# Optimization experiments

Measured on AMD Instinct MI355X. Metric: run time of the kernel, lower is better.

The kernel has to match this reference:

```python
import jax, jax.numpy as jnp
import numpy as np

IN_FEATURES = 2048
OUT_FEATURES = 4096
NUM_SHIFTS = 10  # perms


def setup_inputs() -> dict:
    key = jax.random.key(0)
    kx, kw = jax.random.split(key)
    x = jax.random.normal(kx, (4, 2048, IN_FEATURES), dtype=jnp.float32)
    # nn.Linear weight: (out_features, in_features), Kaiming-uniform-ish init
    bound = 1.0 / np.sqrt(IN_FEATURES)
    W = jax.random.uniform(kw, (OUT_FEATURES, IN_FEATURES), dtype=jnp.float32,
                           minval=-bound, maxval=bound)
    return {"x": x, "W": W}


def _combined_weight(W):
    # Wt: (in, out). Sum of all weight variants; sum_i(x @ W_i) == x @ sum_i(W_i).
    Wt = W.T
    Weff = Wt + jnp.flip(Wt, axis=0) + jnp.flip(Wt, axis=1)
    for i in range(NUM_SHIFTS // 2):
        Weff = Weff + jnp.roll(Wt, shift=i + 1, axis=1)
        Weff = Weff + jnp.roll(Wt, shift=i + 1, axis=0)
    return Weff  # (in, out)


def reference(x, W):
    # reg_out (x @ W.T) + flipped + rolled variants, collapsed into one GEMM
    Weff = _combined_weight(W)
    return jnp.einsum('bsi,io->bso', x, Weff)
```

## Files before the change

kernel.cpp:

```cpp
#include <hip/hip_runtime.h>
#include <hip/hip_bf16.h>
#include <stdint.h>

#define M_DIM 8192
#define K_DIM 2048
#define N_DIM 4096
#define BM 256
#define BN 256
#define BK 64
#define NT (K_DIM / BK)
#define NITER (NT / 2)

typedef __attribute__((ext_vector_type(8))) short bf16x8;
typedef __attribute__((ext_vector_type(4))) float f32x4;

__device__ __forceinline__ unsigned short f2bfu(float f) {
    __hip_bfloat16 h = __float2bfloat16(f);
    return __builtin_bit_cast(unsigned short, h);
}

__global__ __launch_bounds__(256) void prep_fused(const float* __restrict__ x,
                                                  const float* __restrict__ W,
                                                  unsigned short* __restrict__ xb,
                                                  unsigned short* __restrict__ wt) {
    const int bid = blockIdx.x;
    if (bid < N_DIM / 2) {
        __shared__ float row0[K_DIM];
        __shared__ float row1[K_DIM];
        const int o0 = bid * 2;
        const float* w0 = W + (size_t)o0 * K_DIM;
        const float* w1 = W + (size_t)(o0 + 1) * K_DIM;
#pragma unroll
        for (int t = 0; t < 2; ++t) {
            ((float4*)row0)[threadIdx.x + 256 * t] = ((const float4*)w0)[threadIdx.x + 256 * t];
            ((float4*)row1)[threadIdx.x + 256 * t] = ((const float4*)w1)[threadIdx.x + 256 * t];
        }
        __syncthreads();

        const float* rF0 = W + (size_t)(N_DIM - 1 - o0) * K_DIM;
        const float* rF1 = W + (size_t)(N_DIM - 2 - o0) * K_DIM;
        const float* rm1 = W + (size_t)((o0 - 1) & (N_DIM - 1)) * K_DIM;
        const float* rm2 = W + (size_t)((o0 - 2) & (N_DIM - 1)) * K_DIM;
        const float* rm3 = W + (size_t)((o0 - 3) & (N_DIM - 1)) * K_DIM;
        const float* rm4 = W + (size_t)((o0 - 4) & (N_DIM - 1)) * K_DIM;
        const float* rm5 = W + (size_t)((o0 - 5) & (N_DIM - 1)) * K_DIM;
        unsigned short* wo0 = wt + (size_t)o0 * K_DIM;
        unsigned short* wo1 = wo0 + K_DIM;

#pragma unroll
        for (int t = 0; t < 2; ++t) {
            const int i0 = (threadIdx.x + 256 * t) * 4;
            const float4 vF0 = *(const float4*)(rF0 + i0);
            const float4 vF1 = *(const float4*)(rF1 + i0);
            const float4 v1  = *(const float4*)(rm1 + i0);
            const float4 v2  = *(const float4*)(rm2 + i0);
            const float4 v3  = *(const float4*)(rm3 + i0);
            const float4 v4  = *(const float4*)(rm4 + i0);
            const float4 v5  = *(const float4*)(rm5 + i0);
            ushort4 ov0, ov1;
#pragma unroll
            for (int j = 0; j < 4; ++j) {
                const int i = i0 + j;
                float s0 = row0[i] + row0[K_DIM - 1 - i]
                         + row0[(i - 1) & (K_DIM - 1)] + row0[(i - 2) & (K_DIM - 1)]
                         + row0[(i - 3) & (K_DIM - 1)] + row0[(i - 4) & (K_DIM - 1)]
                         + row0[(i - 5) & (K_DIM - 1)];
                s0 += (&vF0.x)[j] + (&v1.x)[j] + (&v2.x)[j]
                    + (&v3.x)[j] + (&v4.x)[j] + (&v5.x)[j];
                (&ov0.x)[j] = f2bfu(s0);

                float s1 = row1[i] + row1[K_DIM - 1 - i]
                         + row1[(i - 1) & (K_DIM - 1)] + row1[(i - 2) & (K_DIM - 1)]
                         + row1[(i - 3) & (K_DIM - 1)] + row1[(i - 4) & (K_DIM - 1)]
                         + row1[(i - 5) & (K_DIM - 1)];
                s1 += (&vF1.x)[j] + row0[i] + (&v1.x)[j] + (&v2.x)[j]
                    + (&v3.x)[j] + (&v4.x)[j];
                (&ov1.x)[j] = f2bfu(s1);
            }
            *(ushort4*)(wo0 + i0) = ov0;
            *(ushort4*)(wo1 + i0) = ov1;
        }
    } else {
        const int idx = (bid - N_DIM / 2) * 256 + threadIdx.x;
        float4 v = ((const float4*)x)[idx];
        ushort4 o;
        o.x = f2bfu(v.x); o.y = f2bfu(v.y); o.z = f2bfu(v.z); o.w = f2bfu(v.w);
        ((ushort4*)xb)[idx] = o;
    }
}

__global__ __launch_bounds__(512, 2) void gemm8p(const unsigned short* __restrict__ Ab,
                                                 const unsigned short* __restrict__ Bt,
                                                 float* __restrict__ C) {
    __shared__ __align__(16) char smem[2 * 65536];

    const int tid  = threadIdx.x;
    const int wave = tid >> 6;
    const int lane = tid & 63;

    const int cpx = 256 >> 3;
    const int wg  = ((int)blockIdx.x & 7) * cpx + ((int)blockIdx.x >> 3);

    const int wr = wave >> 2;
    const int wc = wave & 3;

    const int srow = tid >> 3;
    const int lsw  = (lane & 7) ^ ((lane >> 3) & 7);

    const int r16  = lane & 15;
    const int x7   = lane & 7;
    const int ksl0 = (((lane >> 4)    ) ^ x7) * 16;
    const int ksl1 = (((lane >> 4) | 4) ^ x7) * 16;
    const int aRow = (wr * 128 + r16) * 128;
    const int bRow = (wc * 64  + r16) * 128 + 32768;
    const int crow = (lane >> 4) * 4;
    const int ccol = lane & 15;

    f32x4  acc[8][4];
    bf16x8 b[4][2];
    const unsigned short* gA0;
    const unsigned short* gB0;

#define STAGE_HALF(gbase, opoff, h, t, p) do {                                              \
    char* lds_ = smem + (p) * 65536 + (opoff) + (h) * 16384 + wave * 1024;                  \
    const unsigned short* g_ = (gbase) + (size_t)((h) * 128) * K_DIM + (t) * BK;            \
    __builtin_amdgcn_global_load_lds(                                                        \
        (const __attribute__((address_space(1))) unsigned int*)g_,                           \
        (__attribute__((address_space(3))) unsigned int*)lds_, 16, 0, 0);                    \
    __builtin_amdgcn_global_load_lds(                                                        \
        (const __attribute__((address_space(1))) unsigned int*)(g_ + (size_t)64 * K_DIM),    \
        (__attribute__((address_space(3))) unsigned int*)(lds_ + 8192), 16, 0, 0);           \
} while (0)

#define PHASE(P, Q, STAGE_STMT, VM_STMT) do {                                               \
    const char* base_ = smem + (P) * 65536;                                                 \
    bf16x8 a_[2][2];                                                                        \
    a_[0][0] = *(const bf16x8*)(base_ + aRow + (Q) * 4096 + ksl0);                          \
    a_[0][1] = *(const bf16x8*)(base_ + aRow + (Q) * 4096 + ksl1);                          \
    a_[1][0] = *(const bf16x8*)(base_ + aRow + (Q) * 4096 + 2048 + ksl0);                   \
    a_[1][1] = *(const bf16x8*)(base_ + aRow + (Q) * 4096 + 2048 + ksl1);                   \
    STAGE_STMT;                                                                             \
    __builtin_amdgcn_s_barrier();                                                           \
    asm volatile("s_waitcnt lgkmcnt(0)" ::: "memory");                                      \
    __builtin_amdgcn_sched_barrier(0);                                                      \
    __builtin_amdgcn_s_setprio(1);                                                          \
    _Pragma("unroll")                                                                       \
    for (int fm = 0; fm < 2; ++fm)                                                          \
        _Pragma("unroll")                                                                   \
        for (int fn = 0; fn < 4; ++fn) {                                                    \
            acc[(Q)*2 + fm][fn] = __builtin_amdgcn_mfma_f32_16x16x32_bf16(                  \
                a_[fm][0], b[fn][0], acc[(Q)*2 + fm][fn], 0, 0, 0);                         \
            acc[(Q)*2 + fm][fn] = __builtin_amdgcn_mfma_f32_16x16x32_bf16(                  \
                a_[fm][1], b[fn][1], acc[(Q)*2 + fm][fn], 0, 0, 0);                         \
        }                                                                                   \
    __builtin_amdgcn_s_setprio(0);                                                          \
    VM_STMT;                                                                                \
    __builtin_amdgcn_s_barrier();                                                           \
} while (0)

#define FN_CLUSTER(Q, FN) do {                                                              \
    _Pragma("unroll")                                                                       \
    for (int fm = 0; fm < 2; ++fm) {                                                        \
        acc[(Q)*2 + fm][FN] = __builtin_amdgcn_mfma_f32_16x16x32_bf16(                      \
            a_[fm][0], b[FN][0], acc[(Q)*2 + fm][FN], 0, 0, 0);                             \
        acc[(Q)*2 + fm][FN] = __builtin_amdgcn_mfma_f32_16x16x32_bf16(                      \
            a_[fm][1], b[FN][1], acc[(Q)*2 + fm][FN], 0, 0, 0);                             \
    }                                                                                       \
} while (0)

#define PHASE_B(P, Q, STAGE_STMT, VM_STMT) do {                                             \
    const char* base_ = smem + (P) * 65536;                                                 \
    bf16x8 a_[2][2];                                                                        \
    a_[0][0] = *(const bf16x8*)(base_ + aRow + (Q) * 4096 + ksl0);                          \
    a_[0][1] = *(const bf16x8*)(base_ + aRow + (Q) * 4096 + ksl1);                          \
    a_[1][0] = *(const bf16x8*)(base_ + aRow + (Q) * 4096 + 2048 + ksl0);                   \
    a_[1][1] = *(const bf16x8*)(base_ + aRow + (Q) * 4096 + 2048 + ksl1);                   \
    b[0][0] = *(const bf16x8*)(base_ + bRow + ksl0);                                        \
    b[0][1] = *(const bf16x8*)(base_ + bRow + ksl1);                                        \
    __builtin_amdgcn_sched_barrier(0);                                                      \
    b[1][0] = *(const bf16x8*)(base_ + bRow + 2048 + ksl0);                                 \
    b[1][1] = *(const bf16x8*)(base_ + bRow + 2048 + ksl1);                                 \
    __builtin_amdgcn_sched_barrier(0);                                                      \
    b[2][0] = *(const bf16x8*)(base_ + bRow + 4096 + ksl0);                                 \
    b[2][1] = *(const bf16x8*)(base_ + bRow + 4096 + ksl1);                                 \
    __builtin_amdgcn_sched_barrier(0);                                                      \
    b[3][0] = *(const bf16x8*)(base_ + bRow + 6144 + ksl0);                                 \
    b[3][1] = *(const bf16x8*)(base_ + bRow + 6144 + ksl1);                                 \
    __builtin_amdgcn_sched_barrier(0);                                                      \
    STAGE_STMT;                                                                             \
    __builtin_amdgcn_s_barrier();                                                           \
    asm volatile("s_waitcnt lgkmcnt(6)" ::: "memory");                                      \
    __builtin_amdgcn_sched_barrier(0);                                                      \
    __builtin_amdgcn_s_setprio(1);                                                          \
    FN_CLUSTER(Q, 0);                                                                       \
    __builtin_amdgcn_sched_barrier(0);                                                      \
    asm volatile("s_waitcnt lgkmcnt(4)" ::: "memory");                                      \
    __builtin_amdgcn_sched_barrier(0);                                                      \
    FN_CLUSTER(Q, 1);                                                                       \
    __builtin_amdgcn_sched_barrier(0);                                                      \
    asm volatile("s_waitcnt lgkmcnt(2)" ::: "memory");                                      \
    __builtin_amdgcn_sched_barrier(0);                                                      \
    FN_CLUSTER(Q, 2);                                                                       \
    __builtin_amdgcn_sched_barrier(0);                                                      \
    asm volatile("s_waitcnt lgkmcnt(0)" ::: "memory");                                      \
    __builtin_amdgcn_sched_barrier(0);                                                      \
    FN_CLUSTER(Q, 3);                                                                       \
    __builtin_amdgcn_s_setprio(0);                                                          \
    VM_STMT;                                                                                \
    __builtin_amdgcn_s_barrier();                                                           \
} while (0)

#define PROLOGUE() do {                                                                     \
    STAGE_HALF(gB0, 32768, 0, 0, 0);                                                        \
    STAGE_HALF(gB0, 32768, 1, 0, 0);                                                        \
    STAGE_HALF(gA0, 0,     0, 0, 0);                                                        \
    STAGE_HALF(gA0, 0,     1, 0, 0);                                                        \
    STAGE_HALF(gB0, 32768, 0, 1, 1);                                                        \
    STAGE_HALF(gB0, 32768, 1, 1, 1);                                                        \
    STAGE_HALF(gA0, 0,     0, 1, 1);                                                        \
    asm volatile("s_waitcnt vmcnt(6)" ::: "memory");                                        \
    __builtin_amdgcn_s_barrier();                                                           \
} while (0)

#define KLOOP() do {                                                                        \
    for (int u = 0; u < NITER; ++u) {                                                       \
        const bool last = (u == NITER - 1);                                                 \
        const int  t1 = 2 * u + 1, t2 = 2 * u + 2, t3 = 2 * u + 3;                          \
        PHASE_B(0, 0, { STAGE_HALF(gA0, 0, 1, t1, 1); }, {});                               \
        PHASE(0, 1, { if (!last) STAGE_HALF(gB0, 32768, 0, t2, 0); }, {});                  \
        PHASE(0, 2, { if (!last) STAGE_HALF(gB0, 32768, 1, t2, 0); }, {});                  \
        PHASE(0, 3, { if (!last) STAGE_HALF(gA0, 0, 0, t2, 0); },                           \
              { if (last) asm volatile("s_waitcnt vmcnt(0)" ::: "memory");                  \
                else      asm volatile("s_waitcnt vmcnt(6)" ::: "memory"); });              \
        PHASE_B(1, 0, { if (!last) STAGE_HALF(gA0, 0, 1, t2, 0); }, {});                    \
        PHASE(1, 1, { if (!last) STAGE_HALF(gB0, 32768, 0, t3, 1); }, {});                  \
        PHASE(1, 2, { if (!last) STAGE_HALF(gB0, 32768, 1, t3, 1); }, {});                  \
        PHASE(1, 3, { if (!last) STAGE_HALF(gA0, 0, 0, t3, 1); },                           \
              { if (!last) asm volatile("s_waitcnt vmcnt(6)" ::: "memory"); });             \
    }                                                                                       \
} while (0)

#define CSTORE(Cb) do {                                                                     \
    _Pragma("unroll")                                                                       \
    for (int fm = 0; fm < 8; ++fm)                                                          \
        _Pragma("unroll")                                                                   \
        for (int fn = 0; fn < 4; ++fn)                                                      \
            _Pragma("unroll")                                                               \
            for (int r = 0; r < 4; ++r)                                                     \
                (Cb)[(size_t)(fm * 16 + r) * N_DIM + fn * 16] = acc[fm][fn][r];             \
} while (0)

#define ZERO_ACC() do {                                                                     \
    _Pragma("unroll")                                                                       \
    for (int i_ = 0; i_ < 8; ++i_)                                                          \
        _Pragma("unroll")                                                                   \
        for (int j_ = 0; j_ < 4; ++j_)                                                      \
            acc[i_][j_] = (f32x4){0.f, 0.f, 0.f, 0.f};                                      \
} while (0)

    int bm0 = (wg >> 4) * BM;
    int bn0 = (wg & 15) * BN;
    gA0 = Ab + (size_t)(bm0 + srow) * K_DIM + lsw * 8;
    gB0 = Bt + (size_t)(bn0 + srow) * K_DIM + lsw * 8;
    float* Cb0 = C + (size_t)(bm0 + wr * 128 + crow) * N_DIM + (bn0 + wc * 64 + ccol);

    PROLOGUE();
    ZERO_ACC();
    KLOOP();

    bm0 += 4096;
    gA0 = Ab + (size_t)(bm0 + srow) * K_DIM + lsw * 8;
    float* Cb1 = C + (size_t)(bm0 + wr * 128 + crow) * N_DIM + (bn0 + wc * 64 + ccol);

    PROLOGUE();
    CSTORE(Cb0);
    ZERO_ACC();
    KLOOP();
    CSTORE(Cb1);

#undef CSTORE
#undef ZERO_ACC
#undef KLOOP
#undef PROLOGUE
#undef PHASE_B
#undef FN_CLUSTER
#undef PHASE
#undef STAGE_HALF
}

extern "C" void kernel_launch(void* const* d_in, const int* in_sizes, int n_in,
                              void* d_out, int out_size, void* d_ws, size_t ws_size,
                              hipStream_t stream) {
    const float* x = (const float*)d_in[0];
    const float* W = (const float*)d_in[1];
    float* out = (float*)d_out;

    unsigned short* xb = (unsigned short*)d_ws;
    unsigned short* wt = (unsigned short*)((char*)d_ws + (size_t)M_DIM * K_DIM * 2);

    const int cvt_blocks = (M_DIM * K_DIM) / 4 / 256;
    prep_fused<<<N_DIM / 2 + cvt_blocks, 256, 0, stream>>>(x, W, xb, wt);

    gemm8p<<<256, 512, 0, stream>>>(xb, wt, out);
}
```

Before: 164.0 us.

## Fuse x fp32-to-bf16 conversion into GEMM A-tile loading via registers

Removes the separate pass that converted x to bf16 in a workspace. The GEMM now loads fp32 A tiles into registers, converts them to bf16 and writes them into swizzled LDS, with the load issue and LDS write placed across the pipeline phases. This avoids writing and re-reading a bf16 copy of x. In exchange it doubles A-side global read bytes and adds VGPR pressure and conversion ALU work inside the GEMM loop. It also drops the staggered B-fragment loads of the old PHASE_B variant.

```diff
diff --git a/kernel.cpp b/kernel.cpp
--- a/kernel.cpp
+++ b/kernel.cpp
@@ -19,77 +19,66 @@
     return __builtin_bit_cast(unsigned short, h);
 }
 
-__global__ __launch_bounds__(256) void prep_fused(const float* __restrict__ x,
-                                                  const float* __restrict__ W,
-                                                  unsigned short* __restrict__ xb,
-                                                  unsigned short* __restrict__ wt) {
-    const int bid = blockIdx.x;
-    if (bid < N_DIM / 2) {
-        __shared__ float row0[K_DIM];
-        __shared__ float row1[K_DIM];
-        const int o0 = bid * 2;
-        const float* w0 = W + (size_t)o0 * K_DIM;
-        const float* w1 = W + (size_t)(o0 + 1) * K_DIM;
+__global__ __launch_bounds__(256) void prep_weff(const float* __restrict__ W,
+                                                 unsigned short* __restrict__ wt) {
+    __shared__ float row0[K_DIM];
+    __shared__ float row1[K_DIM];
+    const int o0 = blockIdx.x * 2;
+    const float* w0 = W + (size_t)o0 * K_DIM;
+    const float* w1 = W + (size_t)(o0 + 1) * K_DIM;
 #pragma unroll
-        for (int t = 0; t < 2; ++t) {
-            ((float4*)row0)[threadIdx.x + 256 * t] = ((const float4*)w0)[threadIdx.x + 256 * t];
-            ((float4*)row1)[threadIdx.x + 256 * t] = ((const float4*)w1)[threadIdx.x + 256 * t];
+    for (int t = 0; t < 2; ++t) {
+        ((float4*)row0)[threadIdx.x + 256 * t] = ((const float4*)w0)[threadIdx.x + 256 * t];
+        ((float4*)row1)[threadIdx.x + 256 * t] = ((const float4*)w1)[threadIdx.x + 256 * t];
+    }
+    __syncthreads();
+
+    const float* rF0 = W + (size_t)(N_DIM - 1 - o0) * K_DIM;
+    const float* rF1 = W + (size_t)(N_DIM - 2 - o0) * K_DIM;
+    const float* rm1 = W + (size_t)((o0 - 1) & (N_DIM - 1)) * K_DIM;
+    const float* rm2 = W + (size_t)((o0 - 2) & (N_DIM - 1)) * K_DIM;
+    const float* rm3 = W + (size_t)((o0 - 3) & (N_DIM - 1)) * K_DIM;
+    const float* rm4 = W + (size_t)((o0 - 4) & (N_DIM - 1)) * K_DIM;
+    const float* rm5 = W + (size_t)((o0 - 5) & (N_DIM - 1)) * K_DIM;
+    unsigned short* wo0 = wt + (size_t)o0 * K_DIM;
+    unsigned short* wo1 = wo0 + K_DIM;
+
+#pragma unroll
+    for (int t = 0; t < 2; ++t) {
+        const int i0 = (threadIdx.x + 256 * t) * 4;
+        const float4 vF0 = *(const float4*)(rF0 + i0);
+        const float4 vF1 = *(const float4*)(rF1 + i0);
+        const float4 v1  = *(const float4*)(rm1 + i0);
+        const float4 v2  = *(const float4*)(rm2 + i0);
+        const float4 v3  = *(const float4*)(rm3 + i0);
+        const float4 v4  = *(const float4*)(rm4 + i0);
+        const float4 v5  = *(const float4*)(rm5 + i0);
+        ushort4 ov0, ov1;
+#pragma unroll
+        for (int j = 0; j < 4; ++j) {
+            const int i = i0 + j;
+            float s0 = row0[i] + row0[K_DIM - 1 - i]
+                     + row0[(i - 1) & (K_DIM - 1)] + row0[(i - 2) & (K_DIM - 1)]
+                     + row0[(i - 3) & (K_DIM - 1)] + row0[(i - 4) & (K_DIM - 1)]
+                     + row0[(i - 5) & (K_DIM - 1)];
+            s0 += (&vF0.x)[j] + (&v1.x)[j] + (&v2.x)[j]
+                + (&v3.x)[j] + (&v4.x)[j] + (&v5.x)[j];
+            (&ov0.x)[j] = f2bfu(s0);
+
+            float s1 = row1[i] + row1[K_DIM - 1 - i]
+                     + row1[(i - 1) & (K_DIM - 1)] + row1[(i - 2) & (K_DIM - 1)]
+                     + row1[(i - 3) & (K_DIM - 1)] + row1[(i - 4) & (K_DIM - 1)]
+                     + row1[(i - 5) & (K_DIM - 1)];
+            s1 += (&vF1.x)[j] + row0[i] + (&v1.x)[j] + (&v2.x)[j]
+                + (&v3.x)[j] + (&v4.x)[j];
+            (&ov1.x)[j] = f2bfu(s1);
         }
-        __syncthreads();
-
-        const float* rF0 = W + (size_t)(N_DIM - 1 - o0) * K_DIM;
-        const float* rF1 = W + (size_t)(N_DIM - 2 - o0) * K_DIM;
-        const float* rm1 = W + (size_t)((o0 - 1) & (N_DIM - 1)) * K_DIM;
-        const float* rm2 = W + (size_t)((o0 - 2) & (N_DIM - 1)) * K_DIM;
-        const float* rm3 = W + (size_t)((o0 - 3) & (N_DIM - 1)) * K_DIM;
-        const float* rm4 = W + (size_t)((o0 - 4) & (N_DIM - 1)) * K_DIM;
-        const float* rm5 = W + (size_t)((o0 - 5) & (N_DIM - 1)) * K_DIM;
-        unsigned short* wo0 = wt + (size_t)o0 * K_DIM;
-        unsigned short* wo1 = wo0 + K_DIM;
-
-#pragma unroll
-        for (int t = 0; t < 2; ++t) {
-            const int i0 = (threadIdx.x + 256 * t) * 4;
-            const float4 vF0 = *(const float4*)(rF0 + i0);
-            const float4 vF1 = *(const float4*)(rF1 + i0);
-            const float4 v1  = *(const float4*)(rm1 + i0);
-            const float4 v2  = *(const float4*)(rm2 + i0);
-            const float4 v3  = *(const float4*)(rm3 + i0);
-            const float4 v4  = *(const float4*)(rm4 + i0);
-            const float4 v5  = *(const float4*)(rm5 + i0);
-            ushort4 ov0, ov1;
-#pragma unroll
-            for (int j = 0; j < 4; ++j) {
-                const int i = i0 + j;
-                float s0 = row0[i] + row0[K_DIM - 1 - i]
-                         + row0[(i - 1) & (K_DIM - 1)] + row0[(i - 2) & (K_DIM - 1)]
-                         + row0[(i - 3) & (K_DIM - 1)] + row0[(i - 4) & (K_DIM - 1)]
-                         + row0[(i - 5) & (K_DIM - 1)];
-                s0 += (&vF0.x)[j] + (&v1.x)[j] + (&v2.x)[j]
-                    + (&v3.x)[j] + (&v4.x)[j] + (&v5.x)[j];
-                (&ov0.x)[j] = f2bfu(s0);
-
-                float s1 = row1[i] + row1[K_DIM - 1 - i]
-                         + row1[(i - 1) & (K_DIM - 1)] + row1[(i - 2) & (K_DIM - 1)]
-                         + row1[(i - 3) & (K_DIM - 1)] + row1[(i - 4) & (K_DIM - 1)]
-                         + row1[(i - 5) & (K_DIM - 1)];
-                s1 += (&vF1.x)[j] + row0[i] + (&v1.x)[j] + (&v2.x)[j]
-                    + (&v3.x)[j] + (&v4.x)[j];
-                (&ov1.x)[j] = f2bfu(s1);
-            }
-            *(ushort4*)(wo0 + i0) = ov0;
-            *(ushort4*)(wo1 + i0) = ov1;
-        }
-    } else {
-        const int idx = (bid - N_DIM / 2) * 256 + threadIdx.x;
-        float4 v = ((const float4*)x)[idx];
-        ushort4 o;
-        o.x = f2bfu(v.x); o.y = f2bfu(v.y); o.z = f2bfu(v.z); o.w = f2bfu(v.w);
-        ((ushort4*)xb)[idx] = o;
+        *(ushort4*)(wo0 + i0) = ov0;
+        *(ushort4*)(wo1 + i0) = ov1;
     }
 }
 
-__global__ __launch_bounds__(512, 2) void gemm8p(const unsigned short* __restrict__ Ab,
+__global__ __launch_bounds__(512, 2) void gemm8p(const float* __restrict__ X,
                                                  const unsigned short* __restrict__ Bt,
                                                  float* __restrict__ C) {
     __shared__ __align__(16) char smem[2 * 65536];
@@ -106,6 +95,11 @@
 
     const int srow = tid >> 3;
     const int lsw  = (lane & 7) ^ ((lane >> 3) & 7);
+
+    const int lwr = tid >> 2;
+    const int s0  = (tid & 3) * 2;
+    const int ps0 = (s0     ) ^ (lwr & 7);
+    const int ps1 = (s0 + 1 ) ^ (lwr & 7);
 
     const int r16  = lane & 15;
     const int x7   = lane & 7;
@@ -118,7 +112,9 @@
 
     f32x4  acc[8][4];
     bf16x8 b[4][2];
-    const unsigned short* gA0;
+    float4 a0r0, a0r1, a0r2, a0r3;
+    float4 a1r0, a1r1, a1r2, a1r3;
+    const float* gAx;
     const unsigned short* gB0;
 
 #define STAGE_HALF(gbase, opoff, h, t, p) do {                                              \
@@ -132,9 +128,38 @@
         (__attribute__((address_space(3))) unsigned int*)(lds_ + 8192), 16, 0, 0);           \
 } while (0)
 
-#define PHASE(P, Q, STAGE_STMT, VM_STMT) do {                                               \
+#define A_ISSUE(rp0, rp1, rp2, rp3, h, t) do {                                              \
+    const float* g_ = gAx + (size_t)((h) * 128) * K_DIM + (t) * BK;                         \
+    rp0 = *(const float4*)(g_);                                                             \
+    rp1 = *(const float4*)(g_ + 4);                                                         \
+    rp2 = *(const float4*)(g_ + 8);                                                         \
+    rp3 = *(const float4*)(g_ + 12);                                                        \
+} while (0)
+
+#define A_WRITE(rp0, rp1, rp2, rp3, h, p) do {                                              \
+    unsigned int w0_ = ((unsigned)f2bfu(rp0.y) << 16) | f2bfu(rp0.x);                       \
+    unsigned int w1_ = ((unsigned)f2bfu(rp0.w) << 16) | f2bfu(rp0.z);                       \
+    unsigned int w2_ = ((unsigned)f2bfu(rp1.y) << 16) | f2bfu(rp1.x);                       \
+    unsigned int w3_ = ((unsigned)f2bfu(rp1.w) << 16) | f2bfu(rp1.z);                       \
+    unsigned int w4_ = ((unsigned)f2bfu(rp2.y) << 16) | f2bfu(rp2.x);                       \
+    unsigned int w5_ = ((unsigned)f2bfu(rp2.w) << 16) | f2bfu(rp2.z);                       \
+    unsigned int w6_ = ((unsigned)f2bfu(rp3.y) << 16) | f2bfu(rp3.x);                       \
+    unsigned int w7_ = ((unsigned)f2bfu(rp3.w) << 16) | f2bfu(rp3.z);                       \
+    char* la_ = smem + (p) * 65536 + (h) * 16384 + lwr * 128;                               \
+    *(uint4*)(la_ + ps0 * 16) = (uint4){w0_, w1_, w2_, w3_};                                \
+    *(uint4*)(la_ + ps1 * 16) = (uint4){w4_, w5_, w6_, w7_};                                \
+} while (0)
+
+#define PHASE(P, Q, LOADB, STAGE_STMT, VM_STMT) do {                                        \
     const char* base_ = smem + (P) * 65536;                                                 \
     bf16x8 a_[2][2];                                                                        \
+    if (LOADB) {                                                                            \
+        _Pragma("unroll")                                                                   \
+        for (int fn = 0; fn < 4; ++fn) {                                                    \
+            b[fn][0] = *(const bf16x8*)(base_ + bRow + fn * 2048 + ksl0);                   \
+            b[fn][1] = *(const bf16x8*)(base_ + bRow + fn * 2048 + ksl1);                   \
+        }                                                                                   \
+    }                                                                                       \
     a_[0][0] = *(const bf16x8*)(base_ + aRow + (Q) * 4096 + ksl0);                          \
     a_[0][1] = *(const bf16x8*)(base_ + aRow + (Q) * 4096 + ksl1);                          \
     a_[1][0] = *(const bf16x8*)(base_ + aRow + (Q) * 4096 + 2048 + ksl0);                   \
@@ -158,67 +183,18 @@
     __builtin_amdgcn_s_barrier();                                                           \
 } while (0)
 
-#define FN_CLUSTER(Q, FN) do {                                                              \
-    _Pragma("unroll")                                                                       \
-    for (int fm = 0; fm < 2; ++fm) {                                                        \
-        acc[(Q)*2 + fm][FN] = __builtin_amdgcn_mfma_f32_16x16x32_bf16(                      \
-            a_[fm][0], b[FN][0], acc[(Q)*2 + fm][FN], 0, 0, 0);                             \
-        acc[(Q)*2 + fm][FN] = __builtin_amdgcn_mfma_f32_16x16x32_bf16(                      \
-            a_[fm][1], b[FN][1], acc[(Q)*2 + fm][FN], 0, 0, 0);                             \
-    }                                                                                       \
-} while (0)
-
-#define PHASE_B(P, Q, STAGE_STMT, VM_STMT) do {                                             \
-    const char* base_ = smem + (P) * 65536;                                                 \
-    bf16x8 a_[2][2];                                                                        \
-    a_[0][0] = *(const bf16x8*)(base_ + aRow + (Q) * 4096 + ksl0);                          \
-    a_[0][1] = *(const bf16x8*)(base_ + aRow + (Q) * 4096 + ksl1);                          \
-    a_[1][0] = *(const bf16x8*)(base_ + aRow + (Q) * 4096 + 2048 + ksl0);                   \
-    a_[1][1] = *(const bf16x8*)(base_ + aRow + (Q) * 4096 + 2048 + ksl1);                   \
-    b[0][0] = *(const bf16x8*)(base_ + bRow + ksl0);                                        \
-    b[0][1] = *(const bf16x8*)(base_ + bRow + ksl1);                                        \
-    __builtin_amdgcn_sched_barrier(0);                                                      \
-    b[1][0] = *(const bf16x8*)(base_ + bRow + 2048 + ksl0);                                 \
-    b[1][1] = *(const bf16x8*)(base_ + bRow + 2048 + ksl1);                                 \
-    __builtin_amdgcn_sched_barrier(0);                                                      \
-    b[2][0] = *(const bf16x8*)(base_ + bRow + 4096 + ksl0);                                 \
-    b[2][1] = *(const bf16x8*)(base_ + bRow + 4096 + ksl1);                                 \
-    __builtin_amdgcn_sched_barrier(0);                                                      \
-    b[3][0] = *(const bf16x8*)(base_ + bRow + 6144 + ksl0);                                 \
-    b[3][1] = *(const bf16x8*)(base_ + bRow + 6144 + ksl1);                                 \
-    __builtin_amdgcn_sched_barrier(0);                                                      \
-    STAGE_STMT;                                                                             \
-    __builtin_amdgcn_s_barrier();                                                           \
-    asm volatile("s_waitcnt lgkmcnt(6)" ::: "memory");                                      \
-    __builtin_amdgcn_sched_barrier(0);                                                      \
-    __builtin_amdgcn_s_setprio(1);                                                          \
-    FN_CLUSTER(Q, 0);                                                                       \
-    __builtin_amdgcn_sched_barrier(0);                                                      \
-    asm volatile("s_waitcnt lgkmcnt(4)" ::: "memory");                                      \
-    __builtin_amdgcn_sched_barrier(0);                                                      \
-    FN_CLUSTER(Q, 1);                                                                       \
-    __builtin_amdgcn_sched_barrier(0);                                                      \
-    asm volatile("s_waitcnt lgkmcnt(2)" ::: "memory");                                      \
-    __builtin_amdgcn_sched_barrier(0);                                                      \
-    FN_CLUSTER(Q, 2);                                                                       \
-    __builtin_amdgcn_sched_barrier(0);                                                      \
+#define PROLOGUE() do {                                                                     \
+    A_ISSUE(a0r0, a0r1, a0r2, a0r3, 0, 0);                                       \
+    A_ISSUE(a1r0, a1r1, a1r2, a1r3, 1, 0);                                       \
+    STAGE_HALF(gB0, 32768, 0, 0, 0);                                                        \
+    STAGE_HALF(gB0, 32768, 1, 0, 0);                                             \
+    STAGE_HALF(gB0, 32768, 0, 1, 1);                                                        \
+    STAGE_HALF(gB0, 32768, 1, 1, 1);                                             \
+    asm volatile("s_waitcnt vmcnt(4)" ::: "memory");            \
+    A_WRITE(a0r0, a0r1, a0r2, a0r3, 0, 0);                                                  \
+    A_WRITE(a1r0, a1r1, a1r2, a1r3, 1, 0);                                                  \
     asm volatile("s_waitcnt lgkmcnt(0)" ::: "memory");                                      \
-    __builtin_amdgcn_sched_barrier(0);                                                      \
-    FN_CLUSTER(Q, 3);                                                                       \
-    __builtin_amdgcn_s_setprio(0);                                                          \
-    VM_STMT;                                                                                \
-    __builtin_amdgcn_s_barrier();                                                           \
-} while (0)
-
-#define PROLOGUE() do {                                                                     \
-    STAGE_HALF(gB0, 32768, 0, 0, 0);                                                        \
-    STAGE_HALF(gB0, 32768, 1, 0, 0);                                                        \
-    STAGE_HALF(gA0, 0,     0, 0, 0);                                                        \
-    STAGE_HALF(gA0, 0,     1, 0, 0);                                                        \
-    STAGE_HALF(gB0, 32768, 0, 1, 1);                                                        \
-    STAGE_HALF(gB0, 32768, 1, 1, 1);                                                        \
-    STAGE_HALF(gA0, 0,     0, 1, 1);                                                        \
-    asm volatile("s_waitcnt vmcnt(6)" ::: "memory");                                        \
+    A_ISSUE(a0r0, a0r1, a0r2, a0r3, 0, 1);                                       \
     __builtin_amdgcn_s_barrier();                                                           \
 } while (0)
 
@@ -226,17 +202,24 @@
     for (int u = 0; u < NITER; ++u) {                                                       \
         const bool last = (u == NITER - 1);                                                 \
         const int  t1 = 2 * u + 1, t2 = 2 * u + 2, t3 = 2 * u + 3;                          \
-        PHASE_B(0, 0, { STAGE_HALF(gA0, 0, 1, t1, 1); }, {});                               \
-        PHASE(0, 1, { if (!last) STAGE_HALF(gB0, 32768, 0, t2, 0); }, {});                  \
-        PHASE(0, 2, { if (!last) STAGE_HALF(gB0, 32768, 1, t2, 0); }, {});                  \
-        PHASE(0, 3, { if (!last) STAGE_HALF(gA0, 0, 0, t2, 0); },                           \
+        PHASE(0, 0, 1, { A_ISSUE(a1r0, a1r1, a1r2, a1r3, 1, t1); }, {});                    \
+        PHASE(0, 1, 0, { if (!last) STAGE_HALF(gB0, 32768, 0, t2, 0); }, {});               \
+        PHASE(0, 2, 0, { if (!last) STAGE_HALF(gB0, 32768, 1, t2, 0); },                    \
               { if (last) asm volatile("s_waitcnt vmcnt(0)" ::: "memory");                  \
-                else      asm volatile("s_waitcnt vmcnt(6)" ::: "memory"); });              \
-        PHASE_B(1, 0, { if (!last) STAGE_HALF(gA0, 0, 1, t2, 0); }, {});                    \
-        PHASE(1, 1, { if (!last) STAGE_HALF(gB0, 32768, 0, t3, 1); }, {});                  \
-        PHASE(1, 2, { if (!last) STAGE_HALF(gB0, 32768, 1, t3, 1); }, {});                  \
-        PHASE(1, 3, { if (!last) STAGE_HALF(gA0, 0, 0, t3, 1); },                           \
-              { if (!last) asm volatile("s_waitcnt vmcnt(6)" ::: "memory"); });             \
+                else      asm volatile("s_waitcnt vmcnt(4)" ::: "memory");                  \
+                A_WRITE(a0r0, a0r1, a0r2, a0r3, 0, 1);                                      \
+                A_WRITE(a1r0, a1r1, a1r2, a1r3, 1, 1);                                      \
+                asm volatile("s_waitcnt lgkmcnt(0)" ::: "memory"); });                      \
+        PHASE(0, 3, 0, { if (!last) A_ISSUE(a0r0, a0r1, a0r2, a0r3, 0, t2); }, {});         \
+        PHASE(1, 0, 1, { if (!last) A_ISSUE(a1r0, a1r1, a1r2, a1r3, 1, t2); }, {});         \
+        PHASE(1, 1, 0, { if (!last) STAGE_HALF(gB0, 32768, 0, t3, 1); }, {});               \
+        PHASE(1, 2, 0, { if (!last) STAGE_HALF(gB0, 32768, 1, t3, 1); },                    \
+              { if (!last) {                                                                \
+                    asm volatile("s_waitcnt vmcnt(4)" ::: "memory");                        \
+                    A_WRITE(a0r0, a0r1, a0r2, a0r3, 0, 0);                                  \
+                    A_WRITE(a1r0, a1r1, a1r2, a1r3, 1, 0);                                  \
+                    asm volatile("s_waitcnt lgkmcnt(0)" ::: "memory"); } });                \
+        PHASE(1, 3, 0, { if (!last) A_ISSUE(a0r0, a0r1, a0r2, a0r3, 0, t3); }, {});         \
     }                                                                                       \
 } while (0)
 
@@ -260,7 +243,7 @@
 
     int bm0 = (wg >> 4) * BM;
     int bn0 = (wg & 15) * BN;
-    gA0 = Ab + (size_t)(bm0 + srow) * K_DIM + lsw * 8;
+    gAx = X + (size_t)(bm0 + lwr) * K_DIM + (tid & 3) * 16;
     gB0 = Bt + (size_t)(bn0 + srow) * K_DIM + lsw * 8;
     float* Cb0 = C + (size_t)(bm0 + wr * 128 + crow) * N_DIM + (bn0 + wc * 64 + ccol);
 
@@ -269,7 +252,7 @@
     KLOOP();
 
     bm0 += 4096;
-    gA0 = Ab + (size_t)(bm0 + srow) * K_DIM + lsw * 8;
+    gAx = X + (size_t)(bm0 + lwr) * K_DIM + (tid & 3) * 16;
     float* Cb1 = C + (size_t)(bm0 + wr * 128 + crow) * N_DIM + (bn0 + wc * 64 + ccol);
 
     PROLOGUE();
@@ -282,9 +265,9 @@
 #undef ZERO_ACC
 #undef KLOOP
 #undef PROLOGUE
-#undef PHASE_B
-#undef FN_CLUSTER
 #undef PHASE
+#undef A_WRITE
+#undef A_ISSUE
 #undef STAGE_HALF
 }
 
@@ -295,11 +278,8 @@
     const float* W = (const float*)d_in[1];
     float* out = (float*)d_out;
 
-    unsigned short* xb = (unsigned short*)d_ws;
-    unsigned short* wt = (unsigned short*)((char*)d_ws + (size_t)M_DIM * K_DIM * 2);
-
-    const int cvt_blocks = (M_DIM * K_DIM) / 4 / 256;
-    prep_fused<<<N_DIM / 2 + cvt_blocks, 256, 0, stream>>>(x, W, xb, wt);
-
-    gemm8p<<<256, 512, 0, stream>>>(xb, wt, out);
-}
+    unsigned short* wt = (unsigned short*)d_ws;
+
+    prep_weff<<<N_DIM / 2, 256, 0, stream>>>(W, wt);
+    gemm8p<<<256, 512, 0, stream>>>(x, wt, out);
+}
```

New measurement: 221.9 us. 35.3% more time.
